# Optimization experiments

Measured on AMD Instinct MI355X. Metric: run time of the kernel, lower is better.

The kernel has to match this reference:

```python
import jax, jax.numpy as jnp
import numpy as np

B, S, DIN, D, H = 32, 2048, 1024, 512, 8
NC, NM = 19, 10


def _mha(q_in, kv, Wq, bq, Wk, bk, Wv, bv, Wo, bo, add_mask):
    # q_in: [B,S,D]; kv: [K,D] (shared across batch); add_mask: [B,S,K] additive logit bias
    Bq, Sq, Dm = q_in.shape
    dh = Dm // H
    q = (q_in @ Wq + bq).reshape(Bq, Sq, H, dh)
    k = (kv @ Wk + bk).reshape(-1, H, dh)
    v = (kv @ Wv + bv).reshape(-1, H, dh)
    logits = jnp.einsum('bshd,khd->bhsk', q, k) / jnp.sqrt(jnp.float32(dh))
    attn = jax.nn.softmax(logits + add_mask[:, None, :, :], axis=-1)  # [B,H,S,K]
    out = jnp.einsum('bhsk,khd->bshd', attn, v).reshape(Bq, Sq, Dm)
    return out @ Wo + bo


def setup_inputs() -> dict:
    key = jax.random.key(0)
    ks = jax.random.split(key, 32)
    s = 0.02
    p = lambda i, shape: jax.random.normal(ks[i], shape, jnp.float32) * s
    z = lambda: jnp.zeros((D,), jnp.float32)
    return {
        'embeddings': jax.random.normal(ks[0], (B, S, DIN), jnp.float32),
        'embeddings_mask': jax.random.randint(ks[1], (B, S), 0, 2, jnp.int32),
        'post_mask': jax.random.randint(ks[2], (B, S), 0, 2, jnp.int32),
        'frame_mask': jax.random.randint(ks[3], (B, S), 0, 2, jnp.int32),
        'cultural_mask': jax.random.randint(ks[4], (B, NC), 0, 2, jnp.int32),
        'moral_mask': jax.random.randint(ks[5], (B, NM), 0, 2, jnp.int32),
        'W_lin': p(6, (DIN, D)), 'b_lin': z(),
        'cultural_table': p(7, (NC, D)), 'moral_table': p(8, (NM, D)),
        'c_Wq': p(9, (D, D)), 'c_bq': z(), 'c_Wk': p(10, (D, D)), 'c_bk': z(),
        'c_Wv': p(11, (D, D)), 'c_bv': z(), 'c_Wo': p(12, (D, D)), 'c_bo': z(),
        'm_Wq': p(13, (D, D)), 'm_bq': z(), 'm_Wk': p(14, (D, D)), 'm_bk': z(),
        'm_Wv': p(15, (D, D)), 'm_bv': z(), 'm_Wo': p(16, (D, D)), 'm_bo': z(),
    }


def reference(embeddings, embeddings_mask, post_mask, frame_mask, cultural_mask, moral_mask,
              W_lin, b_lin, cultural_table, moral_table,
              c_Wq, c_bq, c_Wk, c_bk, c_Wv, c_bv, c_Wo, c_bo,
              m_Wq, m_bq, m_Wk, m_bk, m_Wv, m_bv, m_Wo, m_bo):
    x = embeddings @ W_lin + b_lin  # [B,S,D]
    em = embeddings_mask.astype(jnp.float32)
    pm = em * post_mask.astype(jnp.float32)   # combined post mask [B,S]
    fm = em * frame_mask.astype(jnp.float32)  # combined frame mask [B,S]
    cm = cultural_mask.astype(jnp.float32)    # [B,NC]
    mm = moral_mask.astype(jnp.float32)       # [B,NM]
    cw = (c_Wq, c_bq, c_Wk, c_bk, c_Wv, c_bv, c_Wo, c_bo)
    mw = (m_Wq, m_bq, m_Wk, m_bk, m_Wv, m_bv, m_Wo, m_bo)
    # cultural branch: two stacked cross-attentions, float masks are ADDED to logits
    fc = _mha(x, cultural_table, *cw, fm[:, :, None] + cm[:, None, :])
    pc = _mha(fc, cultural_table, *cw, pm[:, :, None] + cm[:, None, :])
    post_cultural = pc.sum(axis=1) / pm.sum(axis=1, keepdims=True)
    # moral branch
    fmo = _mha(x, moral_table, *mw, fm[:, :, None] + mm[:, None, :])
    pmo = _mha(fmo, moral_table, *mw, pm[:, :, None] + mm[:, None, :])
    post_moral = pmo.sum(axis=1) / pm.sum(axis=1, keepdims=True)
    pooled = post_cultural - post_moral
    return post_cultural, pooled
```

## Files before the change

### kernel.cpp

```cpp
#include <hip/hip_runtime.h>
#include <math.h>

typedef __bf16 bf16;
typedef __bf16 bf16x8 __attribute__((ext_vector_type(8)));
typedef float floatx4 __attribute__((ext_vector_type(4)));

#define S_LEN 2048
#define BATCH 32
#define NHEAD 8
#define KC 19
#define KM 10
#define HKC 152
#define HKM 80
#define NTOT 232
#define NPAD 256

static __device__ __forceinline__ bf16x8 as_b8(uint4 v) { return __builtin_bit_cast(bf16x8, v); }

__global__ __launch_bounds__(256) void prep1(
    const int* __restrict__ em, const int* __restrict__ pmask,
    const int* __restrict__ cmask, const int* __restrict__ mmask,
    const float* __restrict__ ctab, const float* __restrict__ mtab,
    const float* __restrict__ cWk, const float* __restrict__ cbk,
    const float* __restrict__ cWv, const float* __restrict__ cbv,
    const float* __restrict__ mWk, const float* __restrict__ mbk,
    const float* __restrict__ mWv, const float* __restrict__ mbv,
    float* __restrict__ P, float* __restrict__ A2, float* __restrict__ mb,
    float* __restrict__ k1c, float* __restrict__ v1c,
    float* __restrict__ k1m, float* __restrict__ v1m,
    bf16* __restrict__ GT, bf16* __restrict__ Bt,
    float* __restrict__ c1, float* __restrict__ c2)
{
    __shared__ float smem[512];
    const int blk = blockIdx.x, tid = threadIdx.x;

    if (blk < 32) {
        int* red = (int*)smem;
        int b = blk;
        int s = 0;
        for (int i = tid; i < S_LEN; i += 256) s += em[b*S_LEN+i] * pmask[b*S_LEN+i];
        red[tid] = s; __syncthreads();
        for (int o = 128; o; o >>= 1) { if (tid < o) red[tid] += red[tid+o]; __syncthreads(); }
        if (tid == 0) P[b] = (float)red[0];
        float v = 0.f;
        if (tid < HKC) v = (float)cmask[b*KC + (tid % KC)];
        else if (tid < NTOT) v = (float)mmask[b*KM + ((tid - HKC) % KM)];
        mb[b*NPAD + tid] = v;
        A2[b*NPAD + tid] = 0.f;
    } else if (blk < 61) {
        int r = blk - 32;
        const float* T;  const float* Wk; const float* bk; const float* Wv; const float* bv;
        float* k1; float* v1; int row;
        if (r < KC) { T = ctab; Wk = cWk; bk = cbk; Wv = cWv; bv = cbv; k1 = k1c; v1 = v1c; row = r; }
        else        { T = mtab; Wk = mWk; bk = mbk; Wv = mWv; bv = mbv; k1 = k1m; v1 = v1m; row = r - KC; }
        for (int i = tid; i < 512; i += 256) smem[i] = T[row*512+i];
        __syncthreads();
        for (int j = tid; j < 512; j += 256) {
            float sk = bk[j], sv = bv[j];
            for (int d = 0; d < 512; d++) { float t = smem[d]; sk += t*Wk[d*512+j]; sv += t*Wv[d*512+j]; }
            k1[row*512+j] = sk; v1[row*512+j] = sv;
        }
    } else {
        int z = blk - 61;
        for (int i = tid; i < 16384; i += 256) GT[z*16384 + i] = (bf16)0.f;
        for (int i = tid; i < 6144; i += 256) Bt[(size_t)NTOT*1024 + z*6144 + i] = (bf16)0.f;
        if (z == 0) { c1[tid] = 0.f; c2[tid] = 0.f; }
    }
}

__global__ __launch_bounds__(256) void prep2(
    const float* __restrict__ cWq, const float* __restrict__ mWq,
    const float* __restrict__ k1c, const float* __restrict__ v1c,
    const float* __restrict__ k1m, const float* __restrict__ v1m,
    const float* __restrict__ cWo, const float* __restrict__ mWo,
    float* __restrict__ MqTd, float* __restrict__ W2)
{
    __shared__ float smem[15872];
    const int blk = blockIdx.x, tid = threadIdx.x;

    if (blk < 512) {
        int D = blk;
        for (int i = tid; i < 9728; i += 256) smem[i] = k1c[i];
        for (int i = tid; i < 5120; i += 256) smem[9728+i] = k1m[i];
        for (int i = tid; i < 512; i += 256) {
            smem[14848+i] = cWq[(size_t)D*512+i];
            smem[15360+i] = mWq[(size_t)D*512+i];
        }
        __syncthreads();
        if (tid < HKC) {
            int h = tid / KC, k = tid % KC;
            const float* kr = smem + k*512 + h*64;
            float mq = 0.f;
            #pragma unroll 16
            for (int d = 0; d < 64; d++) mq += smem[14848 + h*64 + d] * kr[d];
            MqTd[D*NPAD + tid] = mq;
        }
        if (tid < HKM) {
            int h = tid / KM, k = tid % KM;
            const float* kr = smem + 9728 + k*512 + h*64;
            float mq = 0.f;
            #pragma unroll 16
            for (int d = 0; d < 64; d++) mq += smem[15360 + h*64 + d] * kr[d];
            MqTd[D*NPAD + HKC + tid] = mq;
        }
    } else {
        int n = blk - 512;
        const float* v1; const float* Wo; int h, k;
        if (n < HKC) { v1 = v1c; Wo = cWo; h = n / KC; k = n % KC; }
        else         { v1 = v1m; Wo = mWo; h = (n-HKC) / KM; k = (n-HKC) % KM; }
        if (tid < 64) smem[tid] = v1[k*512 + h*64 + tid];
        __syncthreads();
        for (int j = tid; j < 512; j += 256) {
            float s = 0.f;
            #pragma unroll 16
            for (int d = 0; d < 64; d++) s += smem[d] * Wo[(size_t)(h*64+d)*512 + j];
            W2[(size_t)n*512 + j] = s;
        }
    }
}

__global__ __launch_bounds__(256) void prep3(
    const float* __restrict__ W_lin, const float* __restrict__ b_lin,
    const float* __restrict__ MqTd, const float* __restrict__ W2,
    const float* __restrict__ k1c, const float* __restrict__ k1m,
    const float* __restrict__ cbq, const float* __restrict__ mbq,
    const float* __restrict__ cbo, const float* __restrict__ mbo,
    bf16* __restrict__ Bt, bf16* __restrict__ GT, float* __restrict__ c1, float* __restrict__ c2)
{
    __shared__ float smem[4096];
    const int blk = blockIdx.x, tid = threadIdx.x;

    if (blk < NTOT) {
        int n = blk;
        for (int i = tid; i < 512; i += 256) smem[i] = W2[(size_t)n*512 + i];
        __syncthreads();
        if (n < HKC) {
            for (int np = tid; np < HKC; np += 256) {
                float s = 0.f;
                for (int t = 0; t < 512; t++) s += smem[t] * MqTd[t*NPAD + np];
                GT[(size_t)np*NPAD + n] = (bf16)(0.125f*s);
            }
        } else {
            for (int np = tid; np < HKM; np += 256) {
                float s = 0.f;
                for (int t = 0; t < 512; t++) s += smem[t] * MqTd[t*NPAD + HKC + np];
                GT[(size_t)(HKC+np)*NPAD + n] = (bf16)(0.125f*s);
            }
        }
    } else if (blk < 360) {
        int D0 = (blk - NTOT) * 8;
        for (int i = tid; i < 4096; i += 256)
            smem[i] = W_lin[(size_t)(D0 + (i >> 9))*512 + (i & 511)];
        __syncthreads();
        if (tid < NTOT) {
            float acc[8] = {};
            for (int d = 0; d < 512; d++) {
                float m = MqTd[d*NPAD + tid];
                #pragma unroll
                for (int r = 0; r < 8; r++) acc[r] += smem[r*512 + d] * m;
            }
            #pragma unroll
            for (int r = 0; r < 8; r++)
                Bt[(size_t)tid*1024 + D0 + r] = (bf16)(0.125f*acc[r]);
        }
    } else {
        for (int i = tid; i < 512; i += 256) {
            smem[i] = b_lin[i];
            smem[512+i] = cbo[i];
            smem[1024+i] = mbo[i];
        }
        __syncthreads();
        if (tid < NTOT) {
            bool cult = tid < HKC;
            const float* bo_s = cult ? (smem+512) : (smem+1024);
            float sA = 0.f, sB = 0.f;
            for (int D = 0; D < 512; D++) {
                float m = MqTd[D*NPAD + tid];
                sA += smem[D]*m;
                sB += bo_s[D]*m;
            }
            float skq = 0.f;
            if (cult) {
                int h = tid / KC, k = tid % KC;
                for (int d = 0; d < 64; d++) skq += cbq[h*64+d] * k1c[k*512 + h*64 + d];
            } else {
                int nm = tid - HKC, h = nm / KM, k = nm % KM;
                for (int d = 0; d < 64; d++) skq += mbq[h*64+d] * k1m[k*512 + h*64 + d];
            }
            c1[tid] = 0.125f*(sA + skq);
            c2[tid] = 0.125f*(sB + skq);
        }
    }
}

__global__ __launch_bounds__(256, 2) void g12_kernel(const float* __restrict__ emb,
                                                     const bf16* __restrict__ Bt,
                                                     const bf16* __restrict__ GT,
                                                     const float* __restrict__ c1,
                                                     const float* __restrict__ c2,
                                                     const float* __restrict__ mb,
                                                     float* __restrict__ A2)
{
    __shared__ union UU {
        struct { bf16 As[128*40]; bf16 Bs[256*40]; } s;
        bf16 Ls[128*264];
    } u;
    __shared__ float bias1[256], bias2[256];
    const int tid = threadIdx.x;
    const int m0 = blockIdx.x*128, b = blockIdx.x >> 4;
    bias1[tid] = c1[tid] + mb[b*NPAD + tid];
    bias2[tid] = c2[tid] + mb[b*NPAD + tid];
    const int wave = tid >> 6, lane = tid & 63, lr = lane & 15, kg = lane >> 4;
    floatx4 acc[8][4] = {};
    const int arow = tid >> 1, acol = (tid & 1)*16;
    const float* ap = emb + (size_t)(m0 + arow)*1024 + acol;
    bf16* asw = u.s.As + arow*40 + acol;
    const bf16* bp = Bt + (size_t)tid*1024;
    bf16* bsw = u.s.Bs + tid*40;
    const bf16* afp = u.s.As + lr*40 + kg*8;
    const bf16* bfp = u.s.Bs + (wave*64 + lr)*40 + kg*8;

    for (int k0 = 0; k0 < 1024; k0 += 32) {
        float4 f0 = *(const float4*)(ap + k0);
        float4 f1 = *(const float4*)(ap + k0 + 4);
        float4 f2 = *(const float4*)(ap + k0 + 8);
        float4 f3 = *(const float4*)(ap + k0 + 12);
        uint4 b0 = *(const uint4*)(bp + k0);
        uint4 b1 = *(const uint4*)(bp + k0 + 8);
        uint4 b2 = *(const uint4*)(bp + k0 + 16);
        uint4 b3 = *(const uint4*)(bp + k0 + 24);
        __syncthreads();
        bf16x8 p0, p1;
        p0[0]=(bf16)f0.x; p0[1]=(bf16)f0.y; p0[2]=(bf16)f0.z; p0[3]=(bf16)f0.w;
        p0[4]=(bf16)f1.x; p0[5]=(bf16)f1.y; p0[6]=(bf16)f1.z; p0[7]=(bf16)f1.w;
        p1[0]=(bf16)f2.x; p1[1]=(bf16)f2.y; p1[2]=(bf16)f2.z; p1[3]=(bf16)f2.w;
        p1[4]=(bf16)f3.x; p1[5]=(bf16)f3.y; p1[6]=(bf16)f3.z; p1[7]=(bf16)f3.w;
        *(bf16x8*)asw = p0; *(bf16x8*)(asw + 8) = p1;
        *(uint4*)bsw = b0; *(uint4*)(bsw + 8) = b1; *(uint4*)(bsw + 16) = b2; *(uint4*)(bsw + 24) = b3;
        __syncthreads();
        bf16x8 af[8], bfr[4];
        #pragma unroll
        for (int mi = 0; mi < 8; mi++) af[mi] = *(const bf16x8*)(afp + mi*16*40);
        #pragma unroll
        for (int nt = 0; nt < 4; nt++) bfr[nt] = *(const bf16x8*)(bfp + nt*16*40);
        #pragma unroll
        for (int mi = 0; mi < 8; mi++)
            #pragma unroll
            for (int nt = 0; nt < 4; nt++)
                acc[mi][nt] = __builtin_amdgcn_mfma_f32_16x16x32_bf16(af[mi], bfr[nt], acc[mi][nt], 0, 0, 0);
    }
    __syncthreads();
    #pragma unroll
    for (int nt = 0; nt < 4; nt++) {
        int col = wave*64 + nt*16 + lr;
        float bb = bias1[col];
        #pragma unroll
        for (int mi = 0; mi < 8; mi++) {
            int row = mi*16 + kg*4;
            #pragma unroll
            for (int r = 0; r < 4; r++)
                u.Ls[(row + r)*264 + col] = (bf16)(acc[mi][nt][r] + bb);
        }
    }
    __syncthreads();
    {
        int row = tid & 127;
        bf16* Lr = u.Ls + row*264;
        if (tid < 128) {
            for (int h = 0; h < NHEAD; h++) {
                float lv[KC]; float m = -1e30f;
                #pragma unroll
                for (int j = 0; j < KC; j++) { lv[j] = (float)Lr[h*KC + j]; m = fmaxf(m, lv[j]); }
                float s = 0.f;
                #pragma unroll
                for (int j = 0; j < KC; j++) { lv[j] = __expf(lv[j] - m); s += lv[j]; }
                float inv = 1.f / s;
                #pragma unroll
                for (int j = 0; j < KC; j++) Lr[h*KC + j] = (bf16)(lv[j]*inv);
            }
        } else {
            for (int h = 0; h < NHEAD; h++) {
                float lv[KM]; float m = -1e30f;
                #pragma unroll
                for (int j = 0; j < KM; j++) { lv[j] = (float)Lr[HKC + h*KM + j]; m = fmaxf(m, lv[j]); }
                float s = 0.f;
                #pragma unroll
                for (int j = 0; j < KM; j++) { lv[j] = __expf(lv[j] - m); s += lv[j]; }
                float inv = 1.f / s;
                #pragma unroll
                for (int j = 0; j < KM; j++) Lr[HKC + h*KM + j] = (bf16)(lv[j]*inv);
            }
            for (int c = NTOT; c < NPAD; c++) Lr[c] = (bf16)0.f;
        }
    }
    __syncthreads();

    floatx4 acc2[8][4] = {};
    {
        const bf16* afp3 = u.Ls + lr*264 + kg*8;
        const bf16* gt0 = GT + (size_t)(wave*64 + lr)*NPAD + kg*8;
        #pragma unroll 2
        for (int t = 0; t < 8; t++) {
            bf16x8 gbv[4], af3[8];
            #pragma unroll
            for (int nt = 0; nt < 4; nt++) gbv[nt] = *(const bf16x8*)(gt0 + nt*16*NPAD + t*32);
            #pragma unroll
            for (int mi = 0; mi < 8; mi++) af3[mi] = *(const bf16x8*)(afp3 + mi*16*264 + t*32);
            #pragma unroll
            for (int mi = 0; mi < 8; mi++)
                #pragma unroll
                for (int nt = 0; nt < 4; nt++)
                    acc2[mi][nt] = __builtin_amdgcn_mfma_f32_16x16x32_bf16(af3[mi], gbv[nt], acc2[mi][nt], 0, 0, 0);
        }
    }
    __syncthreads();

    #pragma unroll
    for (int nt = 0; nt < 4; nt++) {
        int col = wave*64 + nt*16 + lr;
        float bb = bias2[col];
        #pragma unroll
        for (int mi = 0; mi < 8; mi++) {
            int row = mi*16 + kg*4;
            #pragma unroll
            for (int r = 0; r < 4; r++)
                u.Ls[(row + r)*264 + col] = (bf16)(acc2[mi][nt][r] + bb);
        }
    }
    __syncthreads();
    {
        int row = tid & 127;
        bf16* Lr = u.Ls + row*264;
        if (tid < 128) {
            for (int h = 0; h < NHEAD; h++) {
                float lv[KC]; float m = -1e30f;
                #pragma unroll
                for (int j = 0; j < KC; j++) { lv[j] = (float)Lr[h*KC + j]; m = fmaxf(m, lv[j]); }
                float s = 0.f;
                #pragma unroll
                for (int j = 0; j < KC; j++) { lv[j] = __expf(lv[j] - m); s += lv[j]; }
                float inv = 1.f / s;
                #pragma unroll
                for (int j = 0; j < KC; j++) Lr[h*KC + j] = (bf16)(lv[j]*inv);
            }
        } else {
            for (int h = 0; h < NHEAD; h++) {
                float lv[KM]; float m = -1e30f;
                #pragma unroll
                for (int j = 0; j < KM; j++) { lv[j] = (float)Lr[HKC + h*KM + j]; m = fmaxf(m, lv[j]); }
                float s = 0.f;
                #pragma unroll
                for (int j = 0; j < KM; j++) { lv[j] = __expf(lv[j] - m); s += lv[j]; }
                float inv = 1.f / s;
                #pragma unroll
                for (int j = 0; j < KM; j++) Lr[HKC + h*KM + j] = (bf16)(lv[j]*inv);
            }
        }
    }
    __syncthreads();
    {
        float s = 0.f;
        for (int r = 0; r < 128; r++) s += (float)u.Ls[r*264 + tid];
        if (tid < NTOT) atomicAdd(&A2[b*NPAD + tid], s);
    }
}

__global__ __launch_bounds__(256) void finalize_kernel(const float* __restrict__ A2, const float* __restrict__ W2,
                                                       const float* __restrict__ cbo, const float* __restrict__ mbo,
                                                       const float* __restrict__ P, float* __restrict__ out)
{
    __shared__ float a[NTOT];
    int b = blockIdx.x, tid = threadIdx.x;
    if (tid < NTOT) a[tid] = A2[b*NPAD + tid];
    __syncthreads();
    float invP = 1.f / P[b];
    for (int j = tid; j < 512; j += 256) {
        float pc = 2048.f*cbo[j], pm = 2048.f*mbo[j];
        for (int n = 0; n < HKC; n++) pc += a[n]*W2[n*512 + j];
        for (int n = HKC; n < NTOT; n++) pm += a[n]*W2[n*512 + j];
        out[b*512 + j] = pc*invP;
        out[BATCH*512 + b*512 + j] = (pc - pm)*invP;
    }
}

extern "C" void kernel_launch(void* const* d_in, const int* in_sizes, int n_in,
                              void* d_out, int out_size, void* d_ws, size_t ws_size,
                              hipStream_t stream)
{
    (void)in_sizes; (void)n_in; (void)out_size;
    const float* emb   = (const float*)d_in[0];
    const int* emask   = (const int*)d_in[1];
    const int* pmask   = (const int*)d_in[2];
    const int* cmask   = (const int*)d_in[4];
    const int* mmask   = (const int*)d_in[5];
    const float* W_lin = (const float*)d_in[6];
    const float* b_lin = (const float*)d_in[7];
    const float* ctab  = (const float*)d_in[8];
    const float* mtab  = (const float*)d_in[9];
    const float* cWq = (const float*)d_in[10]; const float* cbq = (const float*)d_in[11];
    const float* cWk = (const float*)d_in[12]; const float* cbk = (const float*)d_in[13];
    const float* cWv = (const float*)d_in[14]; const float* cbv = (const float*)d_in[15];
    const float* cWo = (const float*)d_in[16]; const float* cbo = (const float*)d_in[17];
    const float* mWq = (const float*)d_in[18]; const float* mbq = (const float*)d_in[19];
    const float* mWk = (const float*)d_in[20]; const float* mbk = (const float*)d_in[21];
    const float* mWv = (const float*)d_in[22]; const float* mbv = (const float*)d_in[23];
    const float* mWo = (const float*)d_in[24]; const float* mbo = (const float*)d_in[25];
    float* outp = (float*)d_out;

    if (ws_size < 40000000UL) return;

    char* ws = (char*)d_ws;
    size_t o = 0;
    bf16* Bt    = (bf16*)(ws + o); o += 256*1024*2;
    bf16* GT    = (bf16*)(ws + o); o += NPAD*NPAD*2;
    float* k1c  = (float*)(ws + o); o += KC*512*4;
    float* v1c  = (float*)(ws + o); o += KC*512*4;
    float* k1m  = (float*)(ws + o); o += KM*512*4;
    float* v1m  = (float*)(ws + o); o += KM*512*4;
    float* MqTd = (float*)(ws + o); o += (size_t)512*NPAD*4;
    float* W2   = (float*)(ws + o); o += (size_t)NTOT*512*4;
    float* c1   = (float*)(ws + o); o += NPAD*4;
    float* c2   = (float*)(ws + o); o += NPAD*4;
    float* mbt  = (float*)(ws + o); o += BATCH*NPAD*4;
    float* P    = (float*)(ws + o); o += 128;
    float* A2   = (float*)(ws + o); o += BATCH*NPAD*4;

    dim3 blk(256);

    prep1<<<dim3(65), blk, 0, stream>>>(emask, pmask, cmask, mmask, ctab, mtab,
                                        cWk, cbk, cWv, cbv, mWk, mbk, mWv, mbv,
                                        P, A2, mbt, k1c, v1c, k1m, v1m, GT, Bt, c1, c2);
    prep2<<<dim3(744), blk, 0, stream>>>(cWq, mWq, k1c, v1c, k1m, v1m, cWo, mWo, MqTd, W2);
    prep3<<<dim3(361), blk, 0, stream>>>(W_lin, b_lin, MqTd, W2, k1c, k1m,
                                         cbq, mbq, cbo, mbo, Bt, GT, c1, c2);
    g12_kernel<<<dim3(512), blk, 0, stream>>>(emb, Bt, GT, c1, c2, mbt, A2);
    finalize_kernel<<<dim3(BATCH), blk, 0, stream>>>(A2, W2, cbo, mbo, P, outp);
}
```

Before: 630.6 us.

## Halve g12 row tile to 64, double K step, spread softmax over all threads

The fused GEMM/softmax kernel now processes 64 rows per block instead of 128, and the grid doubles to 1024 blocks. The K-loop stages 64 columns per iteration, which halves the number of barriers, and launch bounds are raised to 3 blocks per CU to improve occupancy and latency hiding. The row softmax is split across all four waves (four heads each) instead of two halves, so no threads sit idle. In exchange, each block re-reads the full Bt and GT weight matrices for half as many rows, and more atomics are issued into A2.

```diff
diff --git a/kernel.cpp b/kernel.cpp
--- a/kernel.cpp
+++ b/kernel.cpp
@@ -14,8 +14,7 @@
 #define HKM 80
 #define NTOT 232
 #define NPAD 256
-
-static __device__ __forceinline__ bf16x8 as_b8(uint4 v) { return __builtin_bit_cast(bf16x8, v); }
+#define ROWS 64
 
 __global__ __launch_bounds__(256) void prep1(
     const int* __restrict__ em, const int* __restrict__ pmask,
@@ -193,7 +192,7 @@
     }
 }
 
-__global__ __launch_bounds__(256, 2) void g12_kernel(const float* __restrict__ emb,
+__global__ __launch_bounds__(256, 3) void g12_kernel(const float* __restrict__ emb,
                                                      const bf16* __restrict__ Bt,
                                                      const bf16* __restrict__ GT,
                                                      const float* __restrict__ c1,
@@ -202,25 +201,25 @@
                                                      float* __restrict__ A2)
 {
     __shared__ union UU {
-        struct { bf16 As[128*40]; bf16 Bs[256*40]; } s;
-        bf16 Ls[128*264];
+        struct { bf16 As[ROWS*72]; bf16 Bs[256*72]; } s;
+        bf16 Ls[ROWS*264];
     } u;
     __shared__ float bias1[256], bias2[256];
     const int tid = threadIdx.x;
-    const int m0 = blockIdx.x*128, b = blockIdx.x >> 4;
+    const int m0 = blockIdx.x*ROWS, b = blockIdx.x >> 5;
     bias1[tid] = c1[tid] + mb[b*NPAD + tid];
     bias2[tid] = c2[tid] + mb[b*NPAD + tid];
     const int wave = tid >> 6, lane = tid & 63, lr = lane & 15, kg = lane >> 4;
-    floatx4 acc[8][4] = {};
-    const int arow = tid >> 1, acol = (tid & 1)*16;
+    floatx4 acc[4][4] = {};
+    const int arow = tid >> 2, acol = (tid & 3)*16;
     const float* ap = emb + (size_t)(m0 + arow)*1024 + acol;
-    bf16* asw = u.s.As + arow*40 + acol;
+    bf16* asw = u.s.As + arow*72 + acol;
     const bf16* bp = Bt + (size_t)tid*1024;
-    bf16* bsw = u.s.Bs + tid*40;
-    const bf16* afp = u.s.As + lr*40 + kg*8;
-    const bf16* bfp = u.s.Bs + (wave*64 + lr)*40 + kg*8;
-
-    for (int k0 = 0; k0 < 1024; k0 += 32) {
+    bf16* bsw = u.s.Bs + tid*72;
+    const bf16* afp = u.s.As + lr*72 + kg*8;
+    const bf16* bfp = u.s.Bs + (wave*64 + lr)*72 + kg*8;
+
+    for (int k0 = 0; k0 < 1024; k0 += 64) {
         float4 f0 = *(const float4*)(ap + k0);
         float4 f1 = *(const float4*)(ap + k0 + 4);
         float4 f2 = *(const float4*)(ap + k0 + 8);
@@ -229,6 +228,10 @@
         uint4 b1 = *(const uint4*)(bp + k0 + 8);
         uint4 b2 = *(const uint4*)(bp + k0 + 16);
         uint4 b3 = *(const uint4*)(bp + k0 + 24);
+        uint4 b4 = *(const uint4*)(bp + k0 + 32);
+        uint4 b5 = *(const uint4*)(bp + k0 + 40);
+        uint4 b6 = *(const uint4*)(bp + k0 + 48);
+        uint4 b7 = *(const uint4*)(bp + k0 + 56);
         __syncthreads();
         bf16x8 p0, p1;
         p0[0]=(bf16)f0.x; p0[1]=(bf16)f0.y; p0[2]=(bf16)f0.z; p0[3]=(bf16)f0.w;
@@ -237,17 +240,21 @@
         p1[4]=(bf16)f3.x; p1[5]=(bf16)f3.y; p1[6]=(bf16)f3.z; p1[7]=(bf16)f3.w;
         *(bf16x8*)asw = p0; *(bf16x8*)(asw + 8) = p1;
         *(uint4*)bsw = b0; *(uint4*)(bsw + 8) = b1; *(uint4*)(bsw + 16) = b2; *(uint4*)(bsw + 24) = b3;
-        __syncthreads();
-        bf16x8 af[8], bfr[4];
+        *(uint4*)(bsw + 32) = b4; *(uint4*)(bsw + 40) = b5; *(uint4*)(bsw + 48) = b6; *(uint4*)(bsw + 56) = b7;
+        __syncthreads();
         #pragma unroll
-        for (int mi = 0; mi < 8; mi++) af[mi] = *(const bf16x8*)(afp + mi*16*40);
-        #pragma unroll
-        for (int nt = 0; nt < 4; nt++) bfr[nt] = *(const bf16x8*)(bfp + nt*16*40);
-        #pragma unroll
-        for (int mi = 0; mi < 8; mi++)
-            #pragma unroll
-            for (int nt = 0; nt < 4; nt++)
-                acc[mi][nt] = __builtin_amdgcn_mfma_f32_16x16x32_bf16(af[mi], bfr[nt], acc[mi][nt], 0, 0, 0);
+        for (int kk = 0; kk < 64; kk += 32) {
+            bf16x8 af[4], bfr[4];
+            #pragma unroll
+            for (int mi = 0; mi < 4; mi++) af[mi] = *(const bf16x8*)(afp + mi*16*72 + kk);
+            #pragma unroll
+            for (int nt = 0; nt < 4; nt++) bfr[nt] = *(const bf16x8*)(bfp + nt*16*72 + kk);
+            #pragma unroll
+            for (int mi = 0; mi < 4; mi++)
+                #pragma unroll
+                for (int nt = 0; nt < 4; nt++)
+                    acc[mi][nt] = __builtin_amdgcn_mfma_f32_16x16x32_bf16(af[mi], bfr[nt], acc[mi][nt], 0, 0, 0);
+        }
     }
     __syncthreads();
     #pragma unroll
@@ -255,7 +262,7 @@
         int col = wave*64 + nt*16 + lr;
         float bb = bias1[col];
         #pragma unroll
-        for (int mi = 0; mi < 8; mi++) {
+        for (int mi = 0; mi < 4; mi++) {
             int row = mi*16 + kg*4;
             #pragma unroll
             for (int r = 0; r < 4; r++)
@@ -264,10 +271,10 @@
     }
     __syncthreads();
     {
-        int row = tid & 127;
+        int row = tid & 63, part = tid >> 6;
         bf16* Lr = u.Ls + row*264;
-        if (tid < 128) {
-            for (int h = 0; h < NHEAD; h++) {
+        if (part < 2) {
+            for (int h = part*4; h < part*4 + 4; h++) {
                 float lv[KC]; float m = -1e30f;
                 #pragma unroll
                 for (int j = 0; j < KC; j++) { lv[j] = (float)Lr[h*KC + j]; m = fmaxf(m, lv[j]); }
@@ -279,7 +286,7 @@
                 for (int j = 0; j < KC; j++) Lr[h*KC + j] = (bf16)(lv[j]*inv);
             }
         } else {
-            for (int h = 0; h < NHEAD; h++) {
+            for (int h = (part-2)*4; h < (part-2)*4 + 4; h++) {
                 float lv[KM]; float m = -1e30f;
                 #pragma unroll
                 for (int j = 0; j < KM; j++) { lv[j] = (float)Lr[HKC + h*KM + j]; m = fmaxf(m, lv[j]); }
@@ -290,24 +297,24 @@
                 #pragma unroll
                 for (int j = 0; j < KM; j++) Lr[HKC + h*KM + j] = (bf16)(lv[j]*inv);
             }
-            for (int c = NTOT; c < NPAD; c++) Lr[c] = (bf16)0.f;
-        }
-    }
-    __syncthreads();
-
-    floatx4 acc2[8][4] = {};
+            if (part == 3) for (int c = NTOT; c < NPAD; c++) Lr[c] = (bf16)0.f;
+        }
+    }
+    __syncthreads();
+
+    floatx4 acc2[4][4] = {};
     {
         const bf16* afp3 = u.Ls + lr*264 + kg*8;
         const bf16* gt0 = GT + (size_t)(wave*64 + lr)*NPAD + kg*8;
         #pragma unroll 2
         for (int t = 0; t < 8; t++) {
-            bf16x8 gbv[4], af3[8];
+            bf16x8 gbv[4], af3[4];
             #pragma unroll
             for (int nt = 0; nt < 4; nt++) gbv[nt] = *(const bf16x8*)(gt0 + nt*16*NPAD + t*32);
             #pragma unroll
-            for (int mi = 0; mi < 8; mi++) af3[mi] = *(const bf16x8*)(afp3 + mi*16*264 + t*32);
-            #pragma unroll
-            for (int mi = 0; mi < 8; mi++)
+            for (int mi = 0; mi < 4; mi++) af3[mi] = *(const bf16x8*)(afp3 + mi*16*264 + t*32);
+            #pragma unroll
+            for (int mi = 0; mi < 4; mi++)
                 #pragma unroll
                 for (int nt = 0; nt < 4; nt++)
                     acc2[mi][nt] = __builtin_amdgcn_mfma_f32_16x16x32_bf16(af3[mi], gbv[nt], acc2[mi][nt], 0, 0, 0);
@@ -320,7 +327,7 @@
         int col = wave*64 + nt*16 + lr;
         float bb = bias2[col];
         #pragma unroll
-        for (int mi = 0; mi < 8; mi++) {
+        for (int mi = 0; mi < 4; mi++) {
             int row = mi*16 + kg*4;
             #pragma unroll
             for (int r = 0; r < 4; r++)
@@ -329,10 +336,10 @@
     }
     __syncthreads();
     {
-        int row = tid & 127;
+        int row = tid & 63, part = tid >> 6;
         bf16* Lr = u.Ls + row*264;
-        if (tid < 128) {
-            for (int h = 0; h < NHEAD; h++) {
+        if (part < 2) {
+            for (int h = part*4; h < part*4 + 4; h++) {
                 float lv[KC]; float m = -1e30f;
                 #pragma unroll
                 for (int j = 0; j < KC; j++) { lv[j] = (float)Lr[h*KC + j]; m = fmaxf(m, lv[j]); }
@@ -344,7 +351,7 @@
                 for (int j = 0; j < KC; j++) Lr[h*KC + j] = (bf16)(lv[j]*inv);
             }
         } else {
-            for (int h = 0; h < NHEAD; h++) {
+            for (int h = (part-2)*4; h < (part-2)*4 + 4; h++) {
                 float lv[KM]; float m = -1e30f;
                 #pragma unroll
                 for (int j = 0; j < KM; j++) { lv[j] = (float)Lr[HKC + h*KM + j]; m = fmaxf(m, lv[j]); }
@@ -360,7 +367,7 @@
     __syncthreads();
     {
         float s = 0.f;
-        for (int r = 0; r < 128; r++) s += (float)u.Ls[r*264 + tid];
+        for (int r = 0; r < ROWS; r++) s += (float)u.Ls[r*264 + tid];
         if (tid < NTOT) atomicAdd(&A2[b*NPAD + tid], s);
     }
 }
@@ -433,6 +440,6 @@
     prep2<<<dim3(744), blk, 0, stream>>>(cWq, mWq, k1c, v1c, k1m, v1m, cWo, mWo, MqTd, W2);
     prep3<<<dim3(361), blk, 0, stream>>>(W_lin, b_lin, MqTd, W2, k1c, k1m,
                                          cbq, mbq, cbo, mbo, Bt, GT, c1, c2);
-    g12_kernel<<<dim3(512), blk, 0, stream>>>(emb, Bt, GT, c1, c2, mbt, A2);
+    g12_kernel<<<dim3(1024), blk, 0, stream>>>(emb, Bt, GT, c1, c2, mbt, A2);
     finalize_kernel<<<dim3(BATCH), blk, 0, stream>>>(A2, W2, cbo, mbo, P, outp);
 }
```

Result: no change. 629.7 us (-0.1%).
